# Kernel optimization log

Hardware: AMD Instinct MI355X
Metric: run time of the kernel (lower is better)

Reference implementation:

```python
import jax, jax.numpy as jnp
import numpy as np
import math

EMBED_DIM = 512
B, H, W = 32, 56, 56


def gen_offsets(c):
    # Faithful port of SpiralFC.gen_offset. offset_groups == c (one (dy, dx) pair
    # per input channel). Only pairs 0..c//2-1 are written by the original code
    # (the loop over num_dims writes the same indices twice); the remaining pairs
    # come from torch.empty and are undefined -> we use 0 for determinism.
    dy = np.zeros(c, dtype=np.float32)
    dx = np.zeros(c, dtype=np.float32)
    num_dim = c // 2
    R = 14.0
    for i in range(num_dim):
        if i <= num_dim // 2:
            r = i * (R / num_dim)
        else:
            r = R - i * (R / num_dim)
        dy[i] = round(r * math.cos(math.pi * i / 16))  # torchvision offset order: (y, x)
        dx[i] = round(r * math.sin(math.pi * i / 16))
    return np.stack([dy, dx], axis=1)  # [C, 2]


def setup_inputs() -> dict:
    key = jax.random.key(0)
    k1, k2, k3 = jax.random.split(key, 3)
    C = EMBED_DIM
    fan_in = C  # 1x1 kernel, groups=1
    x = jax.random.normal(k1, (B, H, W, C), dtype=jnp.float32)
    weight = jax.random.normal(k2, (C, C), dtype=jnp.float32) / np.sqrt(fan_in)
    bias = (jax.random.uniform(k3, (C,), dtype=jnp.float32) - 0.5) * (2.0 / np.sqrt(fan_in))
    offset = jnp.asarray(gen_offsets(C))  # [C, 2] fixed buffer
    return {"x": x, "weight": weight, "bias": bias, "offset": offset}


def _shift_bilinear(xc, dy, dx):
    # xc: [B, C, H, W]; dy, dx: [C] spatially-constant per-channel offsets.
    # Bilinear sampling at (h + dy[c], w + dx[c]) with zero padding, separable
    # along H and W because offsets are constant over space.
    Bn, C, Hn, Wn = xc.shape

    def axis_interp(a, off, axis, size):
        p = jnp.arange(size, dtype=off.dtype)[None, :] + off[:, None]  # [C, size]
        p0 = jnp.floor(p)
        w1 = p - p0                      # [C, size]
        i0 = p0.astype(jnp.int32)
        i1 = i0 + 1

        def gather(idx):
            valid = (idx >= 0) & (idx < size)        # [C, size]
            idxc = jnp.clip(idx, 0, size - 1)
            if axis == 2:
                ind = idxc[None, :, :, None]
                msk = valid[None, :, :, None]
            else:
                ind = idxc[None, :, None, :]
                msk = valid[None, :, None, :]
            return jnp.take_along_axis(a, ind, axis=axis) * msk

        if axis == 2:
            w1b = w1[None, :, :, None]
        else:
            w1b = w1[None, :, None, :]
        return gather(i0) * (1.0 - w1b) + gather(i1) * w1b

    xh = axis_interp(xc, dy, 2, Hn)
    return axis_interp(xh, dx, 3, Wn)


def reference(x, weight, bias, offset):
    # x: [B, H, W, C] (NHWC as in SpiralFC.forward)
    xt = jnp.transpose(x, (0, 3, 1, 2))            # [B, C, H, W]
    xs = _shift_bilinear(xt, offset[:, 0], offset[:, 1])
    out = jnp.einsum('bchw,oc->bohw', xs, weight) + bias[None, :, None, None]
    return out  # [B, C, H, W], matching deform_conv2d output layout
```

## Files before the change

### kernel.cpp

```cpp
#include <hip/hip_runtime.h>
#include <hip/hip_bf16.h>


#define HD 56
#define WD 56
#define HW 3136
#define CCH 512
#define NBATCH 32
#define MTOT (NBATCH * HW)

#define BM 128
#define BN 128
#define BK 64

#define XS_ELEMS ((size_t)MTOT * CCH)
#define XS_BYTES (XS_ELEMS * 2)
#define WB_BYTES ((size_t)CCH * CCH * 2)

typedef __attribute__((ext_vector_type(8))) __bf16 bf16x8;
typedef __attribute__((ext_vector_type(4))) float f32x4;
typedef __attribute__((ext_vector_type(8))) unsigned short ushort8_t;

#define AS1 __attribute__((address_space(1)))
#define AS3 __attribute__((address_space(3)))

__device__ __forceinline__ unsigned short f2bf(float f) {
    __hip_bfloat16 h = __float2bfloat16(f);
    return __builtin_bit_cast(unsigned short, h);
}

__device__ __forceinline__ void load16_lds(const unsigned short* g, unsigned short* l) {
    __builtin_amdgcn_global_load_lds((const AS1 unsigned int*)g,
                                     (AS3 unsigned int*)l, 16, 0, 0);
}

#define SROW_BLOCKS (NBATCH * HD)
#define WGT_BLOCKS (CCH * CCH / 8 / 256)

__global__ __launch_bounds__(256) void shift_row_kernel(
    const float* __restrict__ x,
    const float* __restrict__ wgt,
    const float* __restrict__ offs,
    unsigned short* __restrict__ Xs,
    unsigned short* __restrict__ Wb)
{
    const int tid = threadIdx.x;
    const int bid0 = (int)blockIdx.x;

    if (bid0 >= SROW_BLOCKS) {
        const int e = (bid0 - SROW_BLOCKS) * 256 + tid;
        const float4* src = (const float4*)wgt + (size_t)e * 2;
        float4 a = src[0], b = src[1];
        ushort8_t o;
        o[0] = f2bf(a.x); o[1] = f2bf(a.y); o[2] = f2bf(a.z); o[3] = f2bf(a.w);
        o[4] = f2bf(b.x); o[5] = f2bf(b.y); o[6] = f2bf(b.z); o[7] = f2bf(b.w);
        *(ushort8_t*)(Wb + (size_t)e * 8) = o;
        return;
    }

    const int lb = (bid0 & 7) * (SROW_BLOCKS / 8) + (bid0 >> 3);
    const int b = lb / HD;
    const int y = lb - b * HD;

    __shared__ unsigned short sIn[WD * 256];

    const int c  = tid;
    const int dy = (int)offs[2 * c];
    const int dx = (int)offs[2 * c + 1];
    const int yy = y + dy;
    const bool rowok = (unsigned)yy < (unsigned)HD;
    const float* rowp = x + ((size_t)b * HD + (rowok ? yy : 0)) * WD * CCH + c;

#pragma unroll 4
    for (int xx = 0; xx < WD; xx++) {
        float v = 0.0f;
        if (rowok) v = rowp[(size_t)xx * CCH];
        sIn[xx * 256 + c] = f2bf(v);
    }
    __syncthreads();

    unsigned short* orow = Xs + ((size_t)b * HW + (size_t)y * WD) * CCH;
#pragma unroll 4
    for (int xx = 0; xx < WD; xx++) {
        const int xs = xx + dx;
        unsigned short v = 0;
        if ((unsigned)xs < (unsigned)WD) v = sIn[xs * 256 + c];
        orow[(size_t)xx * CCH + c] = v;
    }

    const float* ibase = x + ((size_t)b * HW + (size_t)y * WD) * CCH;
#pragma unroll
    for (int it = 0; it < 14; it++) {
        const int e = it * 256 + tid;
        const int xx = e >> 6;
        const int cq = e & 63;
        const int cc = 256 + cq * 4;
        float4 v = *(const float4*)(ibase + (size_t)xx * CCH + cc);
        ushort4 u;
        u.x = f2bf(v.x); u.y = f2bf(v.y); u.z = f2bf(v.z); u.w = f2bf(v.w);
        *(ushort4*)(orow + (size_t)xx * CCH + cc) = u;
    }
}

__global__ __launch_bounds__(256) void gemm_kernel(
    const unsigned short* __restrict__ Xs,
    const unsigned short* __restrict__ Wb,
    const float* __restrict__ bias,
    float* __restrict__ out)
{
    __shared__ unsigned short sW[BM * BK];
    __shared__ unsigned short sX[BN * BK];
    __shared__ float sBias[BM];

    const int tid = threadIdx.x;
    const int bid0 = (int)blockIdx.x;
    const int bid  = (bid0 & 7) * (3136 / 8) + (bid0 >> 3);
    const int ot = bid & 3;
    const int pt = bid >> 2;
    const int O0 = ot * BM;
    const int P0 = pt * BN;

    if (tid < BM) sBias[tid] = bias[O0 + tid];

    const int w   = tid >> 6;
    const int l   = tid & 63;
    const int q   = l >> 4;
    const int c16 = l & 15;
    const int wo  = w & 1;
    const int wm  = w >> 1;

    const int lc    = (l & 7) ^ ((l >> 3) & 7);
    const int k7    = c16 & 7;
    const int slot0 = q ^ k7;
    const int slot1 = (4 + q) ^ k7;

    f32x4 acc[4][4];
#pragma unroll
    for (int i = 0; i < 4; i++)
#pragma unroll
        for (int j = 0; j < 4; j++) acc[i][j] = (f32x4)0.0f;

    for (int kk = 0; kk < CCH; kk += BK) {
#pragma unroll
        for (int i = 0; i < 4; i++) {
            const int ib = w * 4 + i;
            const int row = ib * 8 + (l >> 3);
            const unsigned short* gW = Wb + (size_t)(O0 + row) * CCH + kk + lc * 8;
            const unsigned short* gX = Xs + (size_t)(P0 + row) * CCH + kk + lc * 8;
            load16_lds(gW, &sW[ib * 512]);
            load16_lds(gX, &sX[ib * 512]);
        }
        __syncthreads();

#pragma unroll
        for (int s = 0; s < 2; s++) {
            const int slot = s ? slot1 : slot0;
            bf16x8 af[4], bf[4];
#pragma unroll
            for (int i = 0; i < 4; i++) {
                const int row = wo * 64 + i * 16 + c16;
                af[i] = *(const bf16x8*)&sW[row * BK + slot * 8];
            }
#pragma unroll
            for (int j = 0; j < 4; j++) {
                const int row = wm * 64 + j * 16 + c16;
                bf[j] = *(const bf16x8*)&sX[row * BK + slot * 8];
            }
#pragma unroll
            for (int i = 0; i < 4; i++)
#pragma unroll
                for (int j = 0; j < 4; j++)
                    acc[i][j] = __builtin_amdgcn_mfma_f32_16x16x32_bf16(
                        af[i], bf[j], acc[i][j], 0, 0, 0);
        }
        __syncthreads();
    }

#pragma unroll
    for (int j = 0; j < 4; j++) {
        const int g = P0 + wm * 64 + j * 16 + c16;
        const int b = g / HW;
        const int p = g - b * HW;
        float* obase = out + (size_t)b * CCH * HW + p;
#pragma unroll
        for (int i = 0; i < 4; i++) {
#pragma unroll
            for (int r = 0; r < 4; r++) {
                const int o_l = wo * 64 + i * 16 + q * 4 + r;
                obase[(size_t)(O0 + o_l) * HW] = acc[i][j][r] + sBias[o_l];
            }
        }
    }
}

#define LDK 72
__global__ __launch_bounds__(256) void spiralfc_fused(
    const float* __restrict__ x, const float* __restrict__ wgt,
    const float* __restrict__ bias, const float* __restrict__ offs,
    float* __restrict__ out)
{
    __shared__ unsigned short sW[BM * LDK];
    __shared__ unsigned short sX[BN * LDK];
    __shared__ int sDy[CCH];
    __shared__ int sDx[CCH];
    __shared__ float sBias[BM];

    const int tid = threadIdx.x;
    const int bid = blockIdx.x;
    const int O0 = (bid & 3) * BM;
    const int P0 = (bid >> 2) * BN;

    for (int k = tid; k < CCH; k += 256) {
        sDy[k] = (int)offs[2 * k];
        sDx[k] = (int)offs[2 * k + 1];
    }
    if (tid < BM) sBias[tid] = bias[O0 + tid];

    const int w = tid >> 6, l = tid & 63, q = l >> 4, c16 = l & 15;
    const int wo = w & 1, wm = w >> 1;

    f32x4 acc[4][4];
#pragma unroll
    for (int i = 0; i < 4; i++)
#pragma unroll
        for (int j = 0; j < 4; j++) acc[i][j] = (f32x4)0.0f;

    const int kcW = tid & 15, orW = tid >> 4;
    __syncthreads();

    for (int kk = 0; kk < CCH; kk += BK) {
#pragma unroll
        for (int ps = 0; ps < 8; ps++) {
            const int o = ps * 16 + orW;
            const float4 wv = *(const float4*)(wgt + (size_t)(O0 + o) * CCH + kk + kcW * 4);
            ushort4 uv;
            uv.x = f2bf(wv.x); uv.y = f2bf(wv.y); uv.z = f2bf(wv.z); uv.w = f2bf(wv.w);
            *(ushort4*)&sW[o * LDK + kcW * 4] = uv;
        }
#pragma unroll 4
        for (int ps = 0; ps < 32; ps++) {
            const int m = ps * 4 + w;
            const int g = P0 + m;
            const int b = g / HW;
            const int p = g - b * HW;
            const int y = p / WD;
            const int xx = p - y * WD;
            const int k = kk + l;
            const int yy = y + sDy[k];
            const int xs = xx + sDx[k];
            float v = 0.0f;
            if ((unsigned)yy < (unsigned)HD && (unsigned)xs < (unsigned)WD)
                v = x[((size_t)b * HW + yy * WD + xs) * CCH + k];
            sX[m * LDK + l] = f2bf(v);
        }
        __syncthreads();
#pragma unroll
        for (int s = 0; s < 2; s++) {
            bf16x8 af[4], bf[4];
#pragma unroll
            for (int i = 0; i < 4; i++)
                af[i] = *(const bf16x8*)&sW[(wo * 64 + i * 16 + c16) * LDK + s * 32 + q * 8];
#pragma unroll
            for (int j = 0; j < 4; j++)
                bf[j] = *(const bf16x8*)&sX[(wm * 64 + j * 16 + c16) * LDK + s * 32 + q * 8];
#pragma unroll
            for (int i = 0; i < 4; i++)
#pragma unroll
                for (int j = 0; j < 4; j++)
                    acc[i][j] = __builtin_amdgcn_mfma_f32_16x16x32_bf16(
                        af[i], bf[j], acc[i][j], 0, 0, 0);
        }
        __syncthreads();
    }
#pragma unroll
    for (int j = 0; j < 4; j++) {
        const int g = P0 + wm * 64 + j * 16 + c16;
        const int b = g / HW;
        const int p = g - b * HW;
        float* obase = out + (size_t)b * CCH * HW + p;
#pragma unroll
        for (int i = 0; i < 4; i++)
#pragma unroll
            for (int r = 0; r < 4; r++) {
                const int o_l = wo * 64 + i * 16 + q * 4 + r;
                obase[(size_t)(O0 + o_l) * HW] = acc[i][j][r] + sBias[o_l];
            }
    }
}

extern "C" void kernel_launch(void* const* d_in, const int* in_sizes, int n_in,
                              void* d_out, int out_size, void* d_ws, size_t ws_size,
                              hipStream_t stream) {
    const float* x    = (const float*)d_in[0];
    const float* wgt  = (const float*)d_in[1];
    const float* bias = (const float*)d_in[2];
    const float* offs = (const float*)d_in[3];
    float* out = (float*)d_out;

    if (ws_size >= XS_BYTES + WB_BYTES) {
        unsigned short* Xs = (unsigned short*)d_ws;
        unsigned short* Wb = (unsigned short*)((char*)d_ws + XS_BYTES);
        shift_row_kernel<<<dim3(SROW_BLOCKS + WGT_BLOCKS), dim3(256), 0, stream>>>(
            x, wgt, offs, Xs, Wb);
        gemm_kernel<<<dim3(3136), dim3(256), 0, stream>>>(Xs, Wb, bias, out);
    } else {
        spiralfc_fused<<<dim3(3136), dim3(256), 0, stream>>>(x, wgt, bias, offs, out);
    }
}
```

Before: 497.9 us.

## Tile shift kernel with row halo in LDS and double-buffer GEMM K loop

The shift pre-pass now stages an 8-row band plus a 7-row halo for 32 channels into LDS, so each input row is read once per band instead of once per output row. Channels that are not shifted are handled by separate plain bf16 copy blocks. The GEMM main loop gains double-buffered LDS stages, so the next K tile is loaded while MFMAs run on the current one. This doubles LDS use in the GEMM and adds halo over-read in the shift kernel.

```diff
diff --git a/kernel.cpp b/kernel.cpp
--- a/kernel.cpp
+++ b/kernel.cpp
@@ -34,10 +34,12 @@
                                      (AS3 unsigned int*)l, 16, 0, 0);
 }
 
-#define SROW_BLOCKS (NBATCH * HD)
+#define HALO_BLOCKS (NBATCH * 7 * 8)
+#define COPY_BLOCKS 1792
 #define WGT_BLOCKS (CCH * CCH / 8 / 256)
-
-__global__ __launch_bounds__(256) void shift_row_kernel(
+#define SH_ROWS 22
+
+__global__ __launch_bounds__(256) void shift_halo_kernel(
     const float* __restrict__ x,
     const float* __restrict__ wgt,
     const float* __restrict__ offs,
@@ -47,8 +49,8 @@
     const int tid = threadIdx.x;
     const int bid0 = (int)blockIdx.x;
 
-    if (bid0 >= SROW_BLOCKS) {
-        const int e = (bid0 - SROW_BLOCKS) * 256 + tid;
+    if (bid0 >= HALO_BLOCKS + COPY_BLOCKS) {
+        const int e = (bid0 - (HALO_BLOCKS + COPY_BLOCKS)) * 256 + tid;
         const float4* src = (const float4*)wgt + (size_t)e * 2;
         float4 a = src[0], b = src[1];
         ushort8_t o;
@@ -58,47 +60,81 @@
         return;
     }
 
-    const int lb = (bid0 & 7) * (SROW_BLOCKS / 8) + (bid0 >> 3);
-    const int b = lb / HD;
-    const int y = lb - b * HD;
-
-    __shared__ unsigned short sIn[WD * 256];
-
-    const int c  = tid;
+    if (bid0 >= HALO_BLOCKS) {
+        const int cb = bid0 - HALO_BLOCKS;
+        const size_t e0 = (size_t)cb * 3584 + tid;
+#pragma unroll
+        for (int bt = 0; bt < 2; bt++) {
+            float4 v[7];
+#pragma unroll
+            for (int t = 0; t < 7; t++) {
+                const size_t e = e0 + (size_t)(bt * 7 + t) * 256;
+                const size_t px = e >> 6;
+                const int cq = (int)(e & 63);
+                v[t] = *(const float4*)(x + px * CCH + 256 + cq * 4);
+            }
+#pragma unroll
+            for (int t = 0; t < 7; t++) {
+                const size_t e = e0 + (size_t)(bt * 7 + t) * 256;
+                const size_t px = e >> 6;
+                const int cq = (int)(e & 63);
+                ushort4 u;
+                u.x = f2bf(v[t].x); u.y = f2bf(v[t].y);
+                u.z = f2bf(v[t].z); u.w = f2bf(v[t].w);
+                *(ushort4*)(Xs + px * CCH + 256 + cq * 4) = u;
+            }
+        }
+        return;
+    }
+
+    const int lb = (bid0 & 7) * (HALO_BLOCKS / 8) + (bid0 >> 3);
+    const int b  = lb / 56;
+    const int r  = lb - b * 56;
+    const int g  = r >> 3;
+    const int s  = r & 7;
+    const int y0 = g * 8;
+    const int c0 = s * 32;
+
+    __shared__ unsigned short sH[SH_ROWS * WD * 32];
+
+    const float* xb = x + (size_t)b * HW * CCH;
+#pragma unroll
+    for (int bt = 0; bt < 11; bt++) {
+        float v[14];
+#pragma unroll
+        for (int t = 0; t < 14; t++) {
+            const int e = (bt * 14 + t) * 256 + tid;
+            const int rloc = e / 1792;
+            const int rem  = e - rloc * 1792;
+            const int yi = y0 - 7 + rloc;
+            v[t] = ((unsigned)yi < (unsigned)HD)
+                 ? xb[((size_t)yi * WD + (rem >> 5)) * CCH + c0 + (rem & 31)]
+                 : 0.0f;
+        }
+#pragma unroll
+        for (int t = 0; t < 14; t++) {
+            const int e = (bt * 14 + t) * 256 + tid;
+            sH[e] = f2bf(v[t]);
+        }
+    }
+    __syncthreads();
+
+    const int ci = tid & 31;
+    const int c  = c0 + ci;
     const int dy = (int)offs[2 * c];
     const int dx = (int)offs[2 * c + 1];
-    const int yy = y + dy;
-    const bool rowok = (unsigned)yy < (unsigned)HD;
-    const float* rowp = x + ((size_t)b * HD + (rowok ? yy : 0)) * WD * CCH + c;
-
-#pragma unroll 4
-    for (int xx = 0; xx < WD; xx++) {
-        float v = 0.0f;
-        if (rowok) v = rowp[(size_t)xx * CCH];
-        sIn[xx * 256 + c] = f2bf(v);
-    }
-    __syncthreads();
-
-    unsigned short* orow = Xs + ((size_t)b * HW + (size_t)y * WD) * CCH;
-#pragma unroll 4
-    for (int xx = 0; xx < WD; xx++) {
-        const int xs = xx + dx;
-        unsigned short v = 0;
-        if ((unsigned)xs < (unsigned)WD) v = sIn[xs * 256 + c];
-        orow[(size_t)xx * CCH + c] = v;
-    }
-
-    const float* ibase = x + ((size_t)b * HW + (size_t)y * WD) * CCH;
-#pragma unroll
-    for (int it = 0; it < 14; it++) {
+#pragma unroll 8
+    for (int it = 0; it < 56; it++) {
         const int e = it * 256 + tid;
-        const int xx = e >> 6;
-        const int cq = e & 63;
-        const int cc = 256 + cq * 4;
-        float4 v = *(const float4*)(ibase + (size_t)xx * CCH + cc);
-        ushort4 u;
-        u.x = f2bf(v.x); u.y = f2bf(v.y); u.z = f2bf(v.z); u.w = f2bf(v.w);
-        *(ushort4*)(orow + (size_t)xx * CCH + cc) = u;
+        const int yloc = e / 1792;
+        const int rem  = e - yloc * 1792;
+        const int px   = rem >> 5;
+        const int yy_loc = yloc + 7 + dy;
+        const int xs = px + dx;
+        unsigned short u = 0;
+        if ((unsigned)xs < (unsigned)WD)
+            u = sH[(yy_loc * WD + xs) * 32 + ci];
+        Xs[((size_t)b * HW + (size_t)(y0 + yloc) * WD + px) * CCH + c] = u;
     }
 }
 
@@ -108,8 +144,8 @@
     const float* __restrict__ bias,
     float* __restrict__ out)
 {
-    __shared__ unsigned short sW[BM * BK];
-    __shared__ unsigned short sX[BN * BK];
+    __shared__ unsigned short sW[2 * BM * BK];
+    __shared__ unsigned short sX[2 * BN * BK];
     __shared__ float sBias[BM];
 
     const int tid = threadIdx.x;
@@ -140,39 +176,51 @@
 #pragma unroll
         for (int j = 0; j < 4; j++) acc[i][j] = (f32x4)0.0f;
 
-    for (int kk = 0; kk < CCH; kk += BK) {
-#pragma unroll
-        for (int i = 0; i < 4; i++) {
-            const int ib = w * 4 + i;
-            const int row = ib * 8 + (l >> 3);
-            const unsigned short* gW = Wb + (size_t)(O0 + row) * CCH + kk + lc * 8;
-            const unsigned short* gX = Xs + (size_t)(P0 + row) * CCH + kk + lc * 8;
-            load16_lds(gW, &sW[ib * 512]);
-            load16_lds(gX, &sX[ib * 512]);
-        }
-        __syncthreads();
-
-#pragma unroll
-        for (int s = 0; s < 2; s++) {
-            const int slot = s ? slot1 : slot0;
-            bf16x8 af[4], bf[4];
-#pragma unroll
-            for (int i = 0; i < 4; i++) {
-                const int row = wo * 64 + i * 16 + c16;
-                af[i] = *(const bf16x8*)&sW[row * BK + slot * 8];
-            }
-#pragma unroll
-            for (int j = 0; j < 4; j++) {
-                const int row = wm * 64 + j * 16 + c16;
-                bf[j] = *(const bf16x8*)&sX[row * BK + slot * 8];
-            }
-#pragma unroll
-            for (int i = 0; i < 4; i++)
-#pragma unroll
-                for (int j = 0; j < 4; j++)
-                    acc[i][j] = __builtin_amdgcn_mfma_f32_16x16x32_bf16(
-                        af[i], bf[j], acc[i][j], 0, 0, 0);
-        }
+#define STAGE(pw, px_, kk_) do {                                              \
+    _Pragma("unroll")                                                         \
+    for (int i_ = 0; i_ < 4; i_++) {                                          \
+        const int ib_  = w * 4 + i_;                                          \
+        const int row_ = ib_ * 8 + (l >> 3);                                  \
+        load16_lds(Wb + (size_t)(O0 + row_) * CCH + (kk_) + lc * 8,           \
+                   (pw) + ib_ * 512);                                         \
+        load16_lds(Xs + (size_t)(P0 + row_) * CCH + (kk_) + lc * 8,           \
+                   (px_) + ib_ * 512);                                        \
+    }                                                                         \
+} while (0)
+
+#define COMPUTE(pw, px_) do {                                                 \
+    _Pragma("unroll")                                                         \
+    for (int s_ = 0; s_ < 2; s_++) {                                          \
+        const int slot_ = s_ ? slot1 : slot0;                                 \
+        bf16x8 pa[4], pb[4];                                                  \
+        _Pragma("unroll")                                                     \
+        for (int i_ = 0; i_ < 4; i_++)                                        \
+            pa[i_] = *(const bf16x8*)&(pw)[(wo * 64 + i_ * 16 + c16) * BK     \
+                                           + slot_ * 8];                      \
+        _Pragma("unroll")                                                     \
+        for (int j_ = 0; j_ < 4; j_++)                                        \
+            pb[j_] = *(const bf16x8*)&(px_)[(wm * 64 + j_ * 16 + c16) * BK    \
+                                            + slot_ * 8];                     \
+        _Pragma("unroll")                                                     \
+        for (int i_ = 0; i_ < 4; i_++)                                        \
+            _Pragma("unroll")                                                 \
+            for (int j_ = 0; j_ < 4; j_++)                                    \
+                acc[i_][j_] = __builtin_amdgcn_mfma_f32_16x16x32_bf16(        \
+                    pa[i_], pb[j_], acc[i_][j_], 0, 0, 0);                    \
+    }                                                                         \
+} while (0)
+
+    STAGE(sW, sX, 0);
+    __syncthreads();
+
+#pragma unroll
+    for (int t = 0; t < 8; t++) {
+        unsigned short* cw = sW + (t & 1) * (BM * BK);
+        unsigned short* cx = sX + (t & 1) * (BN * BK);
+        unsigned short* nw = sW + ((t & 1) ^ 1) * (BM * BK);
+        unsigned short* nx = sX + ((t & 1) ^ 1) * (BN * BK);
+        if (t < 7) STAGE(nw, nx, (t + 1) * BK);
+        COMPUTE(cw, cx);
         __syncthreads();
     }
 
@@ -191,6 +239,8 @@
             }
         }
     }
+#undef STAGE
+#undef COMPUTE
 }
 
 #define LDK 72
@@ -300,8 +350,8 @@
     if (ws_size >= XS_BYTES + WB_BYTES) {
         unsigned short* Xs = (unsigned short*)d_ws;
         unsigned short* Wb = (unsigned short*)((char*)d_ws + XS_BYTES);
-        shift_row_kernel<<<dim3(SROW_BLOCKS + WGT_BLOCKS), dim3(256), 0, stream>>>(
-            x, wgt, offs, Xs, Wb);
+        shift_halo_kernel<<<dim3(HALO_BLOCKS + COPY_BLOCKS + WGT_BLOCKS),
+                            dim3(256), 0, stream>>>(x, wgt, offs, Xs, Wb);
         gemm_kernel<<<dim3(3136), dim3(256), 0, stream>>>(Xs, Wb, bias, out);
     } else {
         spiralfc_fused<<<dim3(3136), dim3(256), 0, stream>>>(x, wgt, bias, offs, out);
```

After: 669.1 us. +34.4%, slower.
